# Performance work log

Measured on AMD Instinct MI355X. Metric: run time of the kernel, lower is better.

Reference implementation:

```python
import jax, jax.numpy as jnp
import numpy as np

NUM_CLASSES = 11
LOW_T, HIGH_T, EPS = 0.1, 0.2, 1e-6
_DN = ('NCHW', 'OIHW', 'NCHW')

# 5-tap Gaussian (kornia Canny defaults: kernel_size=(5,5), sigma=(1,1))
_g = np.exp(-(np.arange(5.0) - 2.0) ** 2 / 2.0); _g /= _g.sum()
GAUSS_1D = jnp.asarray(_g, dtype=jnp.float32)
# Sobel kernels (unnormalized, as used inside kornia Canny): (2,1,3,3) = [gx, gy]
SOBEL = jnp.asarray(np.stack([
    [[-1.0, 0.0, 1.0], [-2.0, 0.0, 2.0], [-1.0, 0.0, 1.0]],
    [[-1.0, -2.0, -1.0], [0.0, 0.0, 0.0], [1.0, 2.0, 1.0]],
])[:, None], dtype=jnp.float32)
# kornia get_canny_nms_kernel: 8 directional (center=+1, neighbor=-1) kernels
_nms = np.zeros((8, 1, 3, 3), np.float32)
_offs = [(1, 2), (0, 2), (0, 1), (0, 0), (1, 0), (2, 0), (2, 1), (2, 2)]
for _i, (_r, _c) in enumerate(_offs):
    _nms[_i, 0, 1, 1] = 1.0
    _nms[_i, 0, _r, _c] = -1.0
NMS_K = jnp.asarray(_nms)
# hysteresis: "any 8-neighbor is strong" == conv with ring-of-ones > 0
_ring = np.ones((1, 1, 3, 3), np.float32); _ring[0, 0, 1, 1] = 0.0
RING_K = jnp.asarray(_ring)


def _conv(x, k, pad):
    return jax.lax.conv_general_dilated(x, k, (1, 1), pad, dimension_numbers=_DN)


def gaussian_blur(x):  # reflect border, separable 5x5
    xp = jnp.pad(x, ((0, 0), (0, 0), (2, 2), (2, 2)), mode='reflect')
    xp = _conv(xp, GAUSS_1D.reshape(1, 1, 5, 1), 'VALID')
    return _conv(xp, GAUSS_1D.reshape(1, 1, 1, 5), 'VALID')


def canny_edges(x):  # x: (N,1,H,W) -> binary thin edges (N,1,H,W), kornia Canny()[1]
    b = gaussian_blur(x)
    bp = jnp.pad(b, ((0, 0), (0, 0), (1, 1), (1, 1)), mode='edge')  # replicate pad
    g = _conv(bp, SOBEL, 'VALID')                 # (N,2,H,W)
    gx, gy = g[:, :1], g[:, 1:]
    mag = jnp.sqrt(gx * gx + gy * gy + EPS)
    ang = jnp.round(jnp.rad2deg(jnp.arctan2(gy, gx)) / 45.0)  # units of 45 deg
    nms = _conv(mag, NMS_K, 'SAME')               # (N,8,H,W)
    pos = jnp.mod(ang, 8.0).astype(jnp.int32)
    neg = jnp.mod(ang + 4.0, 8.0).astype(jnp.int32)
    cp = jnp.take_along_axis(nms, pos, axis=1)
    cn = jnp.take_along_axis(nms, neg, axis=1)
    mag = mag * (jnp.minimum(cp, cn) > 0.0)       # non-max suppression
    edges = (mag > LOW_T) * 0.5 + (mag > HIGH_T) * 0.5  # 0 / weak(0.5) / strong(1)

    def hyst_step(e):
        weak = (e == 0.5).astype(e.dtype)
        strong = (e == 1.0).astype(e.dtype)
        conn = (_conv(strong, RING_K, 'SAME') > 0).astype(e.dtype)
        hyst = conn * weak + strong
        return hyst + (hyst == 0) * weak * 0.5, hyst

    def cond(st):
        return jnp.any(st[0] != st[1])

    def body(st):
        new, _ = hyst_step(st[0])
        return (new, st[0])

    e_fin, _ = jax.lax.while_loop(cond, body, (edges, -jnp.ones_like(edges)))
    return hyst_step(e_fin)[1]  # final binary hysteresis map


def dilate_cross(x):  # kornia dilation with cross kernel, geodesic border (x >= 0)
    xp = jnp.pad(x, ((0, 0), (0, 0), (1, 1), (1, 1)))
    c = xp[:, :, 1:-1, 1:-1]
    up, dn = xp[:, :, :-2, 1:-1], xp[:, :, 2:, 1:-1]
    lf, rt = xp[:, :, 1:-1, :-2], xp[:, :, 1:-1, 2:]
    return jnp.maximum(jnp.maximum(jnp.maximum(c, up), jnp.maximum(dn, lf)), rt)


def boundary_target(gt):
    onehot = (gt[:, None, :, :] == jnp.arange(NUM_CLASSES)[None, :, None, None]).astype(jnp.float32)
    B, C, H, W = onehot.shape
    e = canny_edges(onehot.reshape(B * C, 1, H, W))  # vectorized over the 11-channel loop
    edge_gt = dilate_cross(e).reshape(B, C, H, W)
    return onehot, edge_gt


def setup_inputs() -> dict:
    key = jax.random.key(0)
    k1, k2, k3 = jax.random.split(key, 3)
    pd = jax.random.normal(k1, (8, 11, 512, 512), dtype=jnp.float32)
    gt = jax.random.randint(k2, (8, 512, 512), 0, 11)
    weight = jax.random.uniform(k3, (11,), dtype=jnp.float32)
    return {"pd": pd, "gt": gt, "weight": weight}


def reference(pd, gt, weight):
    onehot, edge_gt = boundary_target(gt)
    pd_prob = jax.nn.log_softmax(pd, axis=1)
    boundary_gt = onehot + 2.0 * edge_gt * onehot
    return -(weight * jnp.sum(pd_prob * boundary_gt, axis=(0, 2, 3))).sum() / onehot.sum()
```

## Files before the change

### kernel.cpp

```cpp
#include <hip/hip_runtime.h>
#include <cstdint>
#include <cmath>

#define HH 512
#define WW 512
#define NB 8
#define NC 11
#define NPIX (HH*WW)
#define NWPR 8
#define NWORDS (HH*NWPR)

typedef unsigned long long u64;
typedef uint32_t u32;

__device__ __forceinline__ int reflect512(int t) {
  t = t < 0 ? -t : t;
  return t > 511 ? 1022 - t : t;
}

__global__ __launch_bounds__(256) void k_onehot(const int* __restrict__ gt,
                                                u64* __restrict__ planes) {
  int wave = (blockIdx.x * 256 + threadIdx.x) >> 6;
  int lane = threadIdx.x & 63;
  for (int j = wave; j < NB*512*8; j += 4096) {
    int img = j >> 12;
    int rw = j & 4095;
    int gv = gt[(size_t)img*NPIX + rw*64 + lane];
    u64 my = 0;
    #pragma unroll
    for (int c = 0; c < NC; ++c) {
      u64 m = __ballot(gv == c);
      if (lane == c) my = m;
    }
    if (lane < NC)
      planes[(size_t)img*NC*NWORDS + (size_t)lane*NWORDS + rw] = my;
  }
}

#define TA 64

__global__ __launch_bounds__(256) void k_edges(const u64* __restrict__ planes,
                                               u64* __restrict__ strongw,
                                               u64* __restrict__ weakw) {
  __shared__ u64 sbits[72][2];
  __shared__ float sb[68*68];
  __shared__ u32 su[68*72];

  const int z = blockIdx.z;
  const int r0 = blockIdx.y * TA, c0 = blockIdx.x * TA;
  const int tid = threadIdx.x;
  const u64* plane = planes + (size_t)z * NWORDS;

  if (tid < 72) {
    int gr = reflect512(r0 + tid - 4);
    const u64* prow = plane + gr*8;
    int wi = c0 >> 6;
    u64 b = prow[wi];
    u64 w0, w1;
    if (c0 == 0) {
      u64 cc = prow[1];
      w0 = (b << 4) | ((__brevll(b) >> 59) & 0xFull);
      w1 = (b >> 60) | (cc << 4);
    } else if (c0 == WW - TA) {
      u64 a = prow[wi-1];
      w0 = (a >> 60) | (b << 4);
      w1 = (b >> 60) | (((__brevll(b) >> 1) & 0xFull) << 4);
    } else {
      u64 a = prow[wi-1];
      u64 cc = prow[wi+1];
      w0 = (a >> 60) | (b << 4);
      w1 = (b >> 60) | (cc << 4);
    }
    sbits[tid][0] = w0;
    sbits[tid][1] = w1;
  }
  __syncthreads();

  const float g0 = 0.054488684549642945f;
  const float g1 = 0.24420134200323332f;
  const float g2 = 0.4026199468942475f;

  float* t1f = (float*)su;
  for (int k = 0; k < 5; ++k) {
    int j = tid + 256*k;
    if (j < 68*18) {
      int row = j / 18;
      int grp = j - row*18;
      int widx = grp >> 4;
      int shift = (grp & 15) * 4;
      u32 sp[5];
      #pragma unroll
      for (int d = 0; d < 5; ++d) {
        u32 nib = (u32)(sbits[row+d][widx] >> shift) & 0xFu;
        sp[d] = (nib * 0x00204081u) & 0x01010101u;
      }
      u32 s04 = sp[0] + sp[4];
      u32 s13 = sp[1] + sp[3];
      u32 s2  = sp[2];
      float4 o;
      float* op = &o.x;
      #pragma unroll
      for (int jj = 0; jj < 4; ++jj) {
        float a  = (float)((s04 >> (8*jj)) & 0xffu);
        float bb = (float)((s13 >> (8*jj)) & 0xffu);
        float d  = (float)((s2  >> (8*jj)) & 0xffu);
        op[jj] = g0*a + g1*bb + g2*d;
      }
      *(float4*)&t1f[row*72 + grp*4] = o;
    }
  }
  __syncthreads();

  for (int k = 0; k < 5; ++k) {
    int q = tid + 256*k;
    if (q < 68*17) {
      int lb = q / 17, lcq = q - lb*17;
      const float* rp = &t1f[lb*72 + lcq*4];
      float4 a = *(const float4*)rp;
      float4 b = *(const float4*)(rp + 4);
      float4 o;
      o.x = g0*(a.x + b.x) + g1*(a.y + a.w) + g2*a.z;
      o.y = g0*(a.y + b.y) + g1*(a.z + b.x) + g2*a.w;
      o.z = g0*(a.z + b.z) + g1*(a.w + b.y) + g2*b.x;
      o.w = g0*(a.w + b.w) + g1*(b.x + b.z) + g2*b.y;
      *(float4*)&sb[lb*68 + lcq*4] = o;
    }
  }
  __syncthreads();

  {
    const bool rb0 = (r0 == 0), rb1 = (r0 == HH-TA);
    const bool cb0 = (c0 == 0), cb1 = (c0 == WW-TA);
    if (rb0 | rb1 | cb0 | cb1) {
      for (int i = tid; i < 528; i += 256) {
        int rr, cc;
        if (i < 272) {
          int rI = i / 68;
          rr = (rI < 2) ? rI : 64 + rI;
          cc = i - rI*68;
        } else {
          int j = i - 272;
          rr = 2 + (j >> 2);
          int cI = j & 3;
          cc = (cI < 2) ? cI : 64 + cI;
        }
        int sr = (rb0 && rr < 2) ? 2 : ((rb1 && rr > 65) ? 65 : rr);
        int sc = (cb0 && cc < 2) ? 2 : ((cb1 && cc > 65) ? 65 : cc);
        if (sr != rr || sc != cc) sb[rr*68 + cc] = sb[sr*68 + sc];
      }
      __syncthreads();
    }
  }

  u32* mg = su;
  for (int k = 0; k < 5; ++k) {
    int idx = tid + 256*k;
    if (idx < 66*16) {
      int row = idx >> 4;
      int g = idx & 15;
      int cbase = g*4;
      const float* p0 = &sb[row*68 + cbase];
      float4 a0 = *(const float4*)(p0);
      float4 b0 = *(const float4*)(p0 + 4);
      float4 a1 = *(const float4*)(p0 + 68);
      float4 b1 = *(const float4*)(p0 + 72);
      float4 a2 = *(const float4*)(p0 + 136);
      float4 b2 = *(const float4*)(p0 + 140);
      float ur[6], vr[6];
      ur[0] = a0.x + 2.f*a1.x + a2.x;  vr[0] = a2.x - a0.x;
      ur[1] = a0.y + 2.f*a1.y + a2.y;  vr[1] = a2.y - a0.y;
      ur[2] = a0.z + 2.f*a1.z + a2.z;  vr[2] = a2.z - a0.z;
      ur[3] = a0.w + 2.f*a1.w + a2.w;  vr[3] = a2.w - a0.w;
      ur[4] = b0.x + 2.f*b1.x + b2.x;  vr[4] = b2.x - b0.x;
      ur[5] = b0.y + 2.f*b1.y + b2.y;  vr[5] = b2.y - b0.y;
      int gm = r0 + row - 1;
      uint4 ov;
      u32* ovp = &ov.x;
      #pragma unroll
      for (int jj = 0; jj < 4; ++jj) {
        float gx = ur[jj+2] - ur[jj];
        float gy = vr[jj] + 2.f*vr[jj+1] + vr[jj+2];
        float gx2 = gx*gx, gy2 = gy*gy;
        float mvf = gx2 + gy2;
        int axis;
        if (gy2 <= 0.17157287525f*gx2) axis = 0;
        else if (gy2 >= 5.82842712475f*gx2) axis = 2;
        else axis = (gx*gy > 0.f) ? 1 : 3;
        int gmc = c0 + cbase + jj - 1;
        u32 bits = (__float_as_uint(mvf) & ~3u) | (u32)axis;
        bool in = ((unsigned)gm < 512u) && ((unsigned)gmc < 512u);
        ovp[jj] = in ? bits : 0u;
      }
      *(uint4*)&mg[row*68 + cbase] = ov;
    }
  }
  if (tid < 132) {
    int row = tid >> 1, col = 64 + (tid & 1);
    const float* p0 = &sb[row*68 + col];
    float b00=p0[0],   b01=p0[1],   b02=p0[2];
    float b10=p0[68],               b12=p0[70];
    float b20=p0[136], b21=p0[137], b22=p0[138];
    float gx = (b02 + 2.f*b12 + b22) - (b00 + 2.f*b10 + b20);
    float gy = (b20 + 2.f*b21 + b22) - (b00 + 2.f*b01 + b02);
    float gx2 = gx*gx, gy2 = gy*gy;
    float mvf = gx2 + gy2;
    int axis;
    if (gy2 <= 0.17157287525f*gx2) axis = 0;
    else if (gy2 >= 5.82842712475f*gx2) axis = 2;
    else axis = (gx*gy > 0.f) ? 1 : 3;
    int gm = r0 + row - 1, gmc = c0 + col - 1;
    u32 bits = (__float_as_uint(mvf) & ~3u) | (u32)axis;
    bool in = ((unsigned)gm < 512u) && ((unsigned)gmc < 512u);
    mg[row*68 + col] = in ? bits : 0u;
  }
  __syncthreads();

  const int lane = tid & 63;
  const int wv = tid >> 6;
  const u32 THS = __float_as_uint(0.039999f);
  const u32 THW = __float_as_uint(0.009999f);
  size_t obase = (size_t)z * NWORDS + (size_t)r0*NWPR + (size_t)(c0 >> 6);
  for (int k = 0; k < 16; ++k) {
    int lr = wv + k*4;
    u32 mw = mg[(lr+1)*68 + (lane+1)];
    u32 m = mw & ~3u;
    int a = mw & 3;
    int dr = ((0x01 >> (2*a)) & 3) - 1;
    int dc = ((0x1A >> (2*a)) & 3) - 1;
    u32 m1 = mg[(lr+1+dr)*68 + (lane+1+dc)] & ~3u;
    u32 m2 = mg[(lr+1-dr)*68 + (lane+1-dc)] & ~3u;
    bool pass = (m > m1) && (m > m2);
    u64 sw = __ballot(pass && m > THS);
    u64 wk = __ballot(pass && m > THW);
    if (lane == 0) {
      strongw[obase + (size_t)lr*NWPR] = sw;
      weakw  [obase + (size_t)lr*NWPR] = wk;
    }
  }
}

__global__ __launch_bounds__(512) void k_hyst(const u64* __restrict__ strongw,
                                              const u64* __restrict__ weakw,
                                              u64* __restrict__ dil) {
  __shared__ u64 btop[8][8];
  __shared__ u64 bbot[8][8];
  __shared__ int gflag;
  const int z = blockIdx.x;
  const int tid = threadIdx.x;
  const int lane = tid & 63;
  const int w = tid >> 6;
  const int row = tid;

  const u64* sg = strongw + (size_t)z * NWORDS + (size_t)row * NWPR;
  const u64* wg = weakw   + (size_t)z * NWORDS + (size_t)row * NWPR;
  u64* dg = dil + (size_t)z * NWORDS + (size_t)row * NWPR;

  u64 S[8], W[8];
  #pragma unroll
  for (int cw = 0; cw < 8; ++cw) { S[cw] = sg[cw]; W[cw] = wg[cw]; }

  if (tid == 0) gflag = 0;
  if (lane == 0) {
    #pragma unroll
    for (int cw = 0; cw < 8; ++cw) btop[w][cw] = S[cw];
  }
  if (lane == 63) {
    #pragma unroll
    for (int cw = 0; cw < 8; ++cw) bbot[w][cw] = S[cw];
  }
  __syncthreads();

  for (int outer = 0; outer < 200; ++outer) {
    u64 up_b[8], dn_b[8];
    #pragma unroll
    for (int cw = 0; cw < 8; ++cw) {
      up_b[cw] = (w > 0) ? bbot[w-1][cw] : 0ull;
      dn_b[cw] = (w < 7) ? btop[w+1][cw] : 0ull;
    }
    int wchg = 0;
    for (int inner = 0; inner < 256; ++inner) {
      u64 v[8], changed = 0;
      #pragma unroll
      for (int cw = 0; cw < 8; ++cw) {
        u64 up = __shfl_up(S[cw], 1, 64);
        if (lane == 0) up = up_b[cw];
        u64 dn = __shfl_down(S[cw], 1, 64);
        if (lane == 63) dn = dn_b[cw];
        v[cw] = up | S[cw] | dn;
      }
      #pragma unroll
      for (int cw = 0; cw < 8; ++cw) {
        u64 vp = (cw > 0) ? v[cw-1] : 0ull;
        u64 vn = (cw < 7) ? v[cw+1] : 0ull;
        u64 D = (v[cw] << 1) | v[cw] | (v[cw] >> 1) | (vp >> 63) | (vn << 63);
        u64 ns = S[cw] | (W[cw] & D);
        changed |= ns ^ S[cw];
        S[cw] = ns;
      }
      if (!__any(changed != 0ull)) break;
      wchg = 1;
    }
    if (wchg && lane == 0) gflag = 1;
    __syncthreads();
    if (lane == 0) {
      #pragma unroll
      for (int cw = 0; cw < 8; ++cw) btop[w][cw] = S[cw];
    }
    if (lane == 63) {
      #pragma unroll
      for (int cw = 0; cw < 8; ++cw) bbot[w][cw] = S[cw];
    }
    int f = gflag;
    __syncthreads();
    if (tid == 0) gflag = 0;
    __syncthreads();
    if (!f) break;
  }

  u64 d[8];
  #pragma unroll
  for (int cw = 0; cw < 8; ++cw) {
    u64 up = __shfl_up(S[cw], 1, 64);
    if (lane == 0) up = (w > 0) ? bbot[w-1][cw] : 0ull;
    u64 dn = __shfl_down(S[cw], 1, 64);
    if (lane == 63) dn = (w < 7) ? btop[w+1][cw] : 0ull;
    d[cw] = S[cw] | (S[cw] << 1) | (S[cw] >> 1) | up | dn;
  }
  #pragma unroll
  for (int cw = 0; cw < 8; ++cw) {
    if (cw > 0) d[cw] |= S[cw-1] >> 63;
    if (cw < 7) d[cw] |= S[cw+1] << 63;
  }
  #pragma unroll
  for (int cw = 0; cw < 8; cw += 2) {
    ulonglong2 v2; v2.x = d[cw]; v2.y = d[cw+1];
    *(ulonglong2*)&dg[cw] = v2;
  }
}

__global__ __launch_bounds__(256) void k_loss(const float* __restrict__ pd,
                                              const int* __restrict__ gt,
                                              const float* __restrict__ wt,
                                              const u64* __restrict__ dil,
                                              double* __restrict__ acc) {
  int t = blockIdx.x * 256 + threadIdx.x;
  const int QP = NPIX / 4;
  int b = t / QP;
  int p = (t - b*QP) * 4;

  int4 g4 = *(const int4*)(gt + (size_t)b*NPIX + p);
  const float* pb = pd + (size_t)b * NC * NPIX + p;

  float s0=0.f,s1=0.f,s2=0.f,s3=0.f;
  float v0=0.f,v1=0.f,v2=0.f,v3=0.f;
  #pragma unroll
  for (int c = 0; c < NC; ++c) {
    float4 x = *(const float4*)(pb + (size_t)c * NPIX);
    if (c == g4.x) v0 = x.x;
    if (c == g4.y) v1 = x.y;
    if (c == g4.z) v2 = x.z;
    if (c == g4.w) v3 = x.w;
    s0 += __expf(x.x);
    s1 += __expf(x.y);
    s2 += __expf(x.z);
    s3 += __expf(x.w);
  }
  const u64* db = dil + (size_t)b * NC * NWORDS;
  int wi = p >> 6, sh = p & 63;
  u64 w0 = db[(size_t)g4.x * NWORDS + wi];
  u64 w1 = db[(size_t)g4.y * NWORDS + wi];
  u64 w2 = db[(size_t)g4.z * NWORDS + wi];
  u64 w3 = db[(size_t)g4.w * NWORDS + wi];
  float e0 = (float)((w0 >> sh) & 1ull);
  float e1 = (float)((w1 >> (sh+1)) & 1ull);
  float e2 = (float)((w2 >> (sh+2)) & 1ull);
  float e3 = (float)((w3 >> (sh+3)) & 1ull);

  float contrib = wt[g4.x]*(v0 - __logf(s0))*(1.f+2.f*e0)
                + wt[g4.y]*(v1 - __logf(s1))*(1.f+2.f*e1)
                + wt[g4.z]*(v2 - __logf(s2))*(1.f+2.f*e2)
                + wt[g4.w]*(v3 - __logf(s3))*(1.f+2.f*e3);

  float sum = contrib;
  #pragma unroll
  for (int o = 32; o > 0; o >>= 1) sum += __shfl_down(sum, o, 64);
  __shared__ float wsum[4];
  if ((threadIdx.x & 63) == 0) wsum[threadIdx.x >> 6] = sum;
  __syncthreads();
  if (threadIdx.x == 0) {
    double d = (double)wsum[0] + (double)wsum[1] + (double)wsum[2] + (double)wsum[3];
    atomicAdd(acc, d);
  }
}

__global__ void k_fin(const double* __restrict__ acc, float* __restrict__ out) {
  if (threadIdx.x == 0 && blockIdx.x == 0)
    out[0] = (float)(-acc[0] / 2097152.0);
}

extern "C" void kernel_launch(void* const* d_in, const int* in_sizes, int n_in,
                              void* d_out, int out_size, void* d_ws, size_t ws_size,
                              hipStream_t stream) {
  const float* pd = (const float*)d_in[0];
  const int*   gt = (const int*)d_in[1];
  const float* wt = (const float*)d_in[2];
  float* out = (float*)d_out;

  double* acc = (double*)d_ws;
  u64* strongw = (u64*)((char*)d_ws + 256);
  u64* weakw   = strongw + (size_t)NB*NC*NWORDS;
  u64* dilw    = weakw   + (size_t)NB*NC*NWORDS;
  u64* planes  = dilw;

  (void)hipMemsetAsync(d_ws, 0, 256, stream);

  k_onehot<<<1024, 256, 0, stream>>>(gt, planes);

  dim3 gA(WW/TA, HH/TA, NB*NC);
  k_edges<<<gA, 256, 0, stream>>>(planes, strongw, weakw);

  k_hyst<<<NB*NC, 512, 0, stream>>>(strongw, weakw, dilw);

  k_loss<<<(NB*NPIX/4)/256, 256, 0, stream>>>(pd, gt, wt, dilw, acc);
  k_fin<<<1, 64, 0, stream>>>(acc, out);
}
```

Measured before the change: 122.5 us.

## Overlap log-softmax with hysteresis, add run-propagation, fuse final reduction

The per-pixel log-softmax term is moved into extra blocks of the hysteresis launch, so the bandwidth-heavy read of pd overlaps with the latency-bound 88-block hysteresis kernel. The result goes to a temporary buffer that the loss kernel reads with the edge bits. Hysteresis now spreads strong seeds along whole horizontal runs of weak pixels in each iteration, using add-carry bit tricks in both directions, which should cut the iteration count. The final division moves into the loss kernel through a last-block atomic counter, removing one launch. The blur loops also get incremental index math instead of divides. The cost is an extra 8 MB write and read of tbuf.

```diff
diff --git a/kernel.cpp b/kernel.cpp
--- a/kernel.cpp
+++ b/kernel.cpp
@@ -9,6 +9,7 @@
 #define NPIX (HH*WW)
 #define NWPR 8
 #define NWORDS (HH*NWPR)
+#define NLOSSB 2048
 
 typedef unsigned long long u64;
 typedef uint32_t u32;
@@ -81,49 +82,54 @@
   const float g2 = 0.4026199468942475f;
 
   float* t1f = (float*)su;
-  for (int k = 0; k < 5; ++k) {
-    int j = tid + 256*k;
-    if (j < 68*18) {
-      int row = j / 18;
-      int grp = j - row*18;
-      int widx = grp >> 4;
-      int shift = (grp & 15) * 4;
-      u32 sp[5];
-      #pragma unroll
-      for (int d = 0; d < 5; ++d) {
-        u32 nib = (u32)(sbits[row+d][widx] >> shift) & 0xFu;
-        sp[d] = (nib * 0x00204081u) & 0x01010101u;
-      }
-      u32 s04 = sp[0] + sp[4];
-      u32 s13 = sp[1] + sp[3];
-      u32 s2  = sp[2];
-      float4 o;
-      float* op = &o.x;
-      #pragma unroll
-      for (int jj = 0; jj < 4; ++jj) {
-        float a  = (float)((s04 >> (8*jj)) & 0xffu);
-        float bb = (float)((s13 >> (8*jj)) & 0xffu);
-        float d  = (float)((s2  >> (8*jj)) & 0xffu);
-        op[jj] = g0*a + g1*bb + g2*d;
-      }
-      *(float4*)&t1f[row*72 + grp*4] = o;
-    }
-  }
-  __syncthreads();
-
-  for (int k = 0; k < 5; ++k) {
-    int q = tid + 256*k;
-    if (q < 68*17) {
-      int lb = q / 17, lcq = q - lb*17;
-      const float* rp = &t1f[lb*72 + lcq*4];
-      float4 a = *(const float4*)rp;
-      float4 b = *(const float4*)(rp + 4);
-      float4 o;
-      o.x = g0*(a.x + b.x) + g1*(a.y + a.w) + g2*a.z;
-      o.y = g0*(a.y + b.y) + g1*(a.z + b.x) + g2*a.w;
-      o.z = g0*(a.z + b.z) + g1*(a.w + b.y) + g2*b.x;
-      o.w = g0*(a.w + b.w) + g1*(b.x + b.z) + g2*b.y;
-      *(float4*)&sb[lb*68 + lcq*4] = o;
+  {
+    int grp = tid % 18, row = tid / 18;
+    for (int k = 0; k < 5; ++k) {
+      if (row < 68) {
+        int widx = grp >> 4;
+        int shift = (grp & 15) * 4;
+        u32 sp[5];
+        #pragma unroll
+        for (int d = 0; d < 5; ++d) {
+          u32 nib = (u32)(sbits[row+d][widx] >> shift) & 0xFu;
+          sp[d] = (nib * 0x00204081u) & 0x01010101u;
+        }
+        u32 s04 = sp[0] + sp[4];
+        u32 s13 = sp[1] + sp[3];
+        u32 s2  = sp[2];
+        float4 o;
+        float* op = &o.x;
+        #pragma unroll
+        for (int jj = 0; jj < 4; ++jj) {
+          float a  = (float)((s04 >> (8*jj)) & 0xffu);
+          float bb = (float)((s13 >> (8*jj)) & 0xffu);
+          float d  = (float)((s2  >> (8*jj)) & 0xffu);
+          op[jj] = g0*a + g1*bb + g2*d;
+        }
+        *(float4*)&t1f[row*72 + grp*4] = o;
+      }
+      grp += 4; row += 14;
+      if (grp >= 18) { grp -= 18; row += 1; }
+    }
+  }
+  __syncthreads();
+
+  {
+    int grp = tid % 17, row = tid / 17;
+    for (int k = 0; k < 5; ++k) {
+      if (row < 68) {
+        const float* rp = &t1f[row*72 + grp*4];
+        float4 a = *(const float4*)rp;
+        float4 b = *(const float4*)(rp + 4);
+        float4 o;
+        o.x = g0*(a.x + b.x) + g1*(a.y + a.w) + g2*a.z;
+        o.y = g0*(a.y + b.y) + g1*(a.z + b.x) + g2*a.w;
+        o.z = g0*(a.z + b.z) + g1*(a.w + b.y) + g2*b.x;
+        o.w = g0*(a.w + b.w) + g1*(b.x + b.z) + g2*b.y;
+        *(float4*)&sb[row*68 + grp*4] = o;
+      }
+      grp += 1; row += 15;
+      if (grp >= 17) { grp -= 17; row += 1; }
     }
   }
   __syncthreads();
@@ -239,14 +245,47 @@
   }
 }
 
-__global__ __launch_bounds__(512) void k_hyst(const u64* __restrict__ strongw,
-                                              const u64* __restrict__ weakw,
-                                              u64* __restrict__ dil) {
+__global__ __launch_bounds__(512) void k_hyst_lse(const u64* __restrict__ strongw,
+                                                  const u64* __restrict__ weakw,
+                                                  u64* __restrict__ dil,
+                                                  const float* __restrict__ pd,
+                                                  const int* __restrict__ gt,
+                                                  const float* __restrict__ wt,
+                                                  float* __restrict__ tbuf) {
+  const int tid = threadIdx.x;
+  if (blockIdx.x >= NB*NC) {
+    int t = (blockIdx.x - NB*NC) * 512 + tid;
+    int b = t >> 16;
+    int p = (t & 65535) * 4;
+    int4 g4 = *(const int4*)(gt + (size_t)b*NPIX + p);
+    const float* pb = pd + (size_t)b * NC * NPIX + p;
+    float s0=0.f,s1=0.f,s2=0.f,s3=0.f;
+    float v0=0.f,v1=0.f,v2=0.f,v3=0.f;
+    #pragma unroll
+    for (int c = 0; c < NC; ++c) {
+      float4 x = *(const float4*)(pb + (size_t)c * NPIX);
+      if (c == g4.x) v0 = x.x;
+      if (c == g4.y) v1 = x.y;
+      if (c == g4.z) v2 = x.z;
+      if (c == g4.w) v3 = x.w;
+      s0 += __expf(x.x);
+      s1 += __expf(x.y);
+      s2 += __expf(x.z);
+      s3 += __expf(x.w);
+    }
+    float4 o;
+    o.x = wt[g4.x] * (v0 - __logf(s0));
+    o.y = wt[g4.y] * (v1 - __logf(s1));
+    o.z = wt[g4.z] * (v2 - __logf(s2));
+    o.w = wt[g4.w] * (v3 - __logf(s3));
+    *(float4*)(tbuf + (size_t)b*NPIX + p) = o;
+    return;
+  }
+
   __shared__ u64 btop[8][8];
   __shared__ u64 bbot[8][8];
   __shared__ int gflag;
   const int z = blockIdx.x;
-  const int tid = threadIdx.x;
   const int lane = tid & 63;
   const int w = tid >> 6;
   const int row = tid;
@@ -255,9 +294,9 @@
   const u64* wg = weakw   + (size_t)z * NWORDS + (size_t)row * NWPR;
   u64* dg = dil + (size_t)z * NWORDS + (size_t)row * NWPR;
 
-  u64 S[8], W[8];
+  u64 S[8], W[8], Wr[8];
   #pragma unroll
-  for (int cw = 0; cw < 8; ++cw) { S[cw] = sg[cw]; W[cw] = wg[cw]; }
+  for (int cw = 0; cw < 8; ++cw) { S[cw] = sg[cw]; W[cw] = wg[cw]; Wr[cw] = __brevll(W[cw]); }
 
   if (tid == 0) gflag = 0;
   if (lane == 0) {
@@ -293,7 +332,11 @@
         u64 vp = (cw > 0) ? v[cw-1] : 0ull;
         u64 vn = (cw < 7) ? v[cw+1] : 0ull;
         u64 D = (v[cw] << 1) | v[cw] | (v[cw] >> 1) | (vp >> 63) | (vn << 63);
-        u64 ns = S[cw] | (W[cw] & D);
+        u64 seeds = W[cw] & D;
+        u64 L = W[cw] & ~(W[cw] + seeds);
+        u64 sr = __brevll(seeds);
+        u64 R = __brevll(Wr[cw] & ~(Wr[cw] + sr));
+        u64 ns = S[cw] | seeds | L | R;
         changed |= ns ^ S[cw];
         S[cw] = ns;
       }
@@ -338,33 +381,18 @@
   }
 }
 
-__global__ __launch_bounds__(256) void k_loss(const float* __restrict__ pd,
+__global__ __launch_bounds__(256) void k_loss(const float* __restrict__ tbuf,
                                               const int* __restrict__ gt,
-                                              const float* __restrict__ wt,
                                               const u64* __restrict__ dil,
-                                              double* __restrict__ acc) {
+                                              double* __restrict__ acc,
+                                              unsigned int* __restrict__ cnt,
+                                              float* __restrict__ out) {
   int t = blockIdx.x * 256 + threadIdx.x;
-  const int QP = NPIX / 4;
-  int b = t / QP;
-  int p = (t - b*QP) * 4;
+  int b = t >> 16;
+  int p = (t & 65535) * 4;
 
   int4 g4 = *(const int4*)(gt + (size_t)b*NPIX + p);
-  const float* pb = pd + (size_t)b * NC * NPIX + p;
-
-  float s0=0.f,s1=0.f,s2=0.f,s3=0.f;
-  float v0=0.f,v1=0.f,v2=0.f,v3=0.f;
-  #pragma unroll
-  for (int c = 0; c < NC; ++c) {
-    float4 x = *(const float4*)(pb + (size_t)c * NPIX);
-    if (c == g4.x) v0 = x.x;
-    if (c == g4.y) v1 = x.y;
-    if (c == g4.z) v2 = x.z;
-    if (c == g4.w) v3 = x.w;
-    s0 += __expf(x.x);
-    s1 += __expf(x.y);
-    s2 += __expf(x.z);
-    s3 += __expf(x.w);
-  }
+  float4 t4 = *(const float4*)(tbuf + (size_t)b*NPIX + p);
   const u64* db = dil + (size_t)b * NC * NWORDS;
   int wi = p >> 6, sh = p & 63;
   u64 w0 = db[(size_t)g4.x * NWORDS + wi];
@@ -376,12 +404,7 @@
   float e2 = (float)((w2 >> (sh+2)) & 1ull);
   float e3 = (float)((w3 >> (sh+3)) & 1ull);
 
-  float contrib = wt[g4.x]*(v0 - __logf(s0))*(1.f+2.f*e0)
-                + wt[g4.y]*(v1 - __logf(s1))*(1.f+2.f*e1)
-                + wt[g4.z]*(v2 - __logf(s2))*(1.f+2.f*e2)
-                + wt[g4.w]*(v3 - __logf(s3))*(1.f+2.f*e3);
-
-  float sum = contrib;
+  float sum = t4.x*(1.f+2.f*e0) + t4.y*(1.f+2.f*e1) + t4.z*(1.f+2.f*e2) + t4.w*(1.f+2.f*e3);
   #pragma unroll
   for (int o = 32; o > 0; o >>= 1) sum += __shfl_down(sum, o, 64);
   __shared__ float wsum[4];
@@ -390,12 +413,13 @@
   if (threadIdx.x == 0) {
     double d = (double)wsum[0] + (double)wsum[1] + (double)wsum[2] + (double)wsum[3];
     atomicAdd(acc, d);
-  }
-}
-
-__global__ void k_fin(const double* __restrict__ acc, float* __restrict__ out) {
-  if (threadIdx.x == 0 && blockIdx.x == 0)
-    out[0] = (float)(-acc[0] / 2097152.0);
+    __threadfence();
+    unsigned int old = atomicAdd(cnt, 1u);
+    if (old == NLOSSB - 1) {
+      double fin = atomicAdd(acc, 0.0);
+      out[0] = (float)(-fin / 2097152.0);
+    }
+  }
 }
 
 extern "C" void kernel_launch(void* const* d_in, const int* in_sizes, int n_in,
@@ -407,9 +431,11 @@
   float* out = (float*)d_out;
 
   double* acc = (double*)d_ws;
+  unsigned int* cnt = (unsigned int*)((char*)d_ws + 16);
   u64* strongw = (u64*)((char*)d_ws + 256);
   u64* weakw   = strongw + (size_t)NB*NC*NWORDS;
   u64* dilw    = weakw   + (size_t)NB*NC*NWORDS;
+  float* tbuf  = (float*)(dilw + (size_t)NB*NC*NWORDS);
   u64* planes  = dilw;
 
   (void)hipMemsetAsync(d_ws, 0, 256, stream);
@@ -419,8 +445,7 @@
   dim3 gA(WW/TA, HH/TA, NB*NC);
   k_edges<<<gA, 256, 0, stream>>>(planes, strongw, weakw);
 
-  k_hyst<<<NB*NC, 512, 0, stream>>>(strongw, weakw, dilw);
-
-  k_loss<<<(NB*NPIX/4)/256, 256, 0, stream>>>(pd, gt, wt, dilw, acc);
-  k_fin<<<1, 64, 0, stream>>>(acc, out);
-}
+  k_hyst_lse<<<NB*NC + 1024, 512, 0, stream>>>(strongw, weakw, dilw, pd, gt, wt, tbuf);
+
+  k_loss<<<NLOSSB, 256, 0, stream>>>(tbuf, gt, dilw, acc, cnt, out);
+}
```

After: 152.2 us. 24.3% more time.
